# Optimization experiments

Hardware: AMD Instinct MI355X
Metric: run time of the kernel (lower is better)

The kernel has to match this reference:

```python
import jax, jax.numpy as jnp
import numpy as np

N_NODES = 50000
N_EDGES = 800000
D = 64
BN_EPS = 1e-5


def setup_inputs() -> dict:
    key = jax.random.key(0)
    ks = jax.random.split(key, 16)
    x = jax.random.normal(ks[0], (N_NODES, D), dtype=jnp.float32)
    edge_index = jax.random.randint(ks[1], (2, N_EDGES), 0, N_NODES, dtype=jnp.int64)
    s = 1.0 / np.sqrt(D)
    def lin(k):
        kw, kb = jax.random.split(k)
        W = jax.random.uniform(kw, (D, D), jnp.float32, -s, s)
        b = jax.random.uniform(kb, (D,), jnp.float32, -s, s)
        return W, b
    W1_0, b1_0 = lin(ks[2])
    W2_0, b2_0 = lin(ks[3])
    W1_1, b1_1 = lin(ks[4])
    W2_1, b2_1 = lin(ks[5])
    return {
        "x": x, "edge_index": edge_index,
        "W1_0": W1_0, "b1_0": b1_0, "g_0": jnp.ones((D,), jnp.float32), "beta_0": jnp.zeros((D,), jnp.float32), "W2_0": W2_0, "b2_0": b2_0,
        "W1_1": W1_1, "b1_1": b1_1, "g_1": jnp.ones((D,), jnp.float32), "beta_1": jnp.zeros((D,), jnp.float32), "W2_1": W2_1, "b2_1": b2_1,
    }


def _gin_layer(x, src, dst, W1, b1, g, beta, W2, b2):
    # GINConv with eps=0: h_i = MLP( x_i + sum_{j->i} x_j )
    agg = jax.ops.segment_sum(x[src], dst, num_segments=N_NODES)  # [N, D]
    h = agg + x
    h = h @ W1 + b1
    # BatchNorm1d (training-mode batch statistics, biased variance)
    mean = jnp.mean(h, axis=0)
    var = jnp.var(h, axis=0)
    h = (h - mean) * jax.lax.rsqrt(var + BN_EPS) * g + beta
    h = jax.nn.relu(h)
    h = jax.nn.relu(h @ W2 + b2)
    return h


def reference(x, edge_index, W1_0, b1_0, g_0, beta_0, W2_0, b2_0,
              W1_1, b1_1, g_1, beta_1, W2_1, b2_1):
    src = edge_index[0]  # message source j
    dst = edge_index[1]  # aggregation target i
    h1 = _gin_layer(x, src, dst, W1_0, b1_0, g_0, beta_0, W2_0, b2_0)
    h2 = _gin_layer(h1, src, dst, W1_1, b1_1, g_1, beta_1, W2_1, b2_1)
    return (h1, h2)
```

## Files before the change

### kernel.cpp

```cpp
#include <hip/hip_runtime.h>
#include <hip/hip_bf16.h>

#define N_NODES 50000
#define N_EDGES 800000
#define DD 64
#define RPB 64
#define GBLOCKS ((N_NODES + RPB - 1) / RPB)
#define MBLOCKS ((N_NODES + 63) / 64)
#define NBUCKET ((N_NODES + 63) / 64)
#define PIDSTRIDE 800
#define NBP (NBUCKET * 8)
#define SCAN_BLOCKS ((N_NODES + 255) / 256)
#define EDGE_BLOCKS (N_EDGES / 256)
#define BN_EPS 1e-5f


__device__ __forceinline__ float bf2f(unsigned short b) {
    return __uint_as_float(((unsigned)b) << 16);
}
__device__ __forceinline__ float loadF(const void* p, int i, int isf) {
    return isf ? ((const float*)p)[i] : bf2f(((const unsigned short*)p)[i]);
}
template<bool ISF>
__device__ __forceinline__ float4 ld4(const void* p, int i) {
    if (ISF) return *reinterpret_cast<const float4*>((const float*)p + i);
    ushort4 u = *reinterpret_cast<const ushort4*>((const unsigned short*)p + i);
    return make_float4(bf2f(u.x), bf2f(u.y), bf2f(u.z), bf2f(u.w));
}
__device__ __forceinline__ void acc8(float4& a, float4& b, uint4 u) {
    a.x += __uint_as_float(u.x << 16);
    a.y += __uint_as_float(u.x & 0xFFFF0000u);
    a.z += __uint_as_float(u.y << 16);
    a.w += __uint_as_float(u.y & 0xFFFF0000u);
    b.x += __uint_as_float(u.z << 16);
    b.y += __uint_as_float(u.z & 0xFFFF0000u);
    b.z += __uint_as_float(u.w << 16);
    b.w += __uint_as_float(u.w & 0xFFFF0000u);
}

__global__ __launch_bounds__(256) void initcast_kernel(
    const void* __restrict__ x, const int* __restrict__ ei,
    int* __restrict__ flags, int* __restrict__ cnt, int* __restrict__ bpcnt,
    unsigned short* __restrict__ xb)
{
    __shared__ int cntF, cntI;
    int t = threadIdx.x;
    if (t == 0) { cntF = 0; cntI = 0; }
    __syncthreads();
    unsigned short wd = ((const unsigned short*)x)[2 * t];
    int e = (wd >> 7) & 0xFF;
    if (e >= 0x70 && e <= 0x8F) atomicAdd(&cntF, 1);
    if (t < 128 && ei[2 * t + 1] == 0) atomicAdd(&cntI, 1);
    __syncthreads();
    int isf = (cntF < 128) ? 1 : 0;
    int i64 = (cntI > 64) ? 1 : 0;

    int gid = blockIdx.x * 256 + t;
    if (blockIdx.x == 0 && t == 0) {
        flags[0] = isf;
        flags[1] = i64;
    }

    {
        int d = i64 ? ei[2 * N_EDGES + 2 * gid] : ei[N_EDGES + gid];
        atomicAdd(cnt + d, 1);
        atomicAdd(bpcnt + (blockIdx.x & 7) * PIDSTRIDE + (d >> 6), 1);
    }

    int i = gid * 8;
    if (i < N_NODES * DD) {
        if (isf) {
            float4 a = *reinterpret_cast<const float4*>((const float*)x + i);
            float4 b = *reinterpret_cast<const float4*>((const float*)x + i + 4);
            ushort4 o0, o1;
            o0.x = __bfloat16_as_ushort(__float2bfloat16(a.x));
            o0.y = __bfloat16_as_ushort(__float2bfloat16(a.y));
            o0.z = __bfloat16_as_ushort(__float2bfloat16(a.z));
            o0.w = __bfloat16_as_ushort(__float2bfloat16(a.w));
            o1.x = __bfloat16_as_ushort(__float2bfloat16(b.x));
            o1.y = __bfloat16_as_ushort(__float2bfloat16(b.y));
            o1.z = __bfloat16_as_ushort(__float2bfloat16(b.z));
            o1.w = __bfloat16_as_ushort(__float2bfloat16(b.w));
            *reinterpret_cast<ushort4*>(xb + i) = o0;
            *reinterpret_cast<ushort4*>(xb + i + 4) = o1;
        } else {
            *reinterpret_cast<uint4*>(xb + i) =
                *reinterpret_cast<const uint4*>((const unsigned short*)x + i);
        }
    }
}

__global__ __launch_bounds__(256) void scanA_kernel(const int* __restrict__ cnt,
                                                    int* __restrict__ off,
                                                    int* __restrict__ bsum) {
    __shared__ int tmp[256];
    int t = threadIdx.x;
    int i = blockIdx.x * 256 + t;
    int v = (i < N_NODES) ? cnt[i] : 0;
    tmp[t] = v;
    __syncthreads();
    #pragma unroll
    for (int d = 1; d < 256; d <<= 1) {
        int u = (t >= d) ? tmp[t - d] : 0;
        __syncthreads();
        tmp[t] += u;
        __syncthreads();
    }
    if (i < N_NODES) off[i] = tmp[t] - v;
    if (t == 255) bsum[blockIdx.x] = tmp[255];
}

__global__ __launch_bounds__(256) void scanC_kernel(const int* __restrict__ bsum,
                                                    int* __restrict__ off) {
    __shared__ int tmp[256];
    int t = threadIdx.x;
    int v = (t < SCAN_BLOCKS) ? bsum[t] : 0;
    tmp[t] = v;
    __syncthreads();
    #pragma unroll
    for (int d = 1; d < 256; d <<= 1) {
        int u = (t >= d) ? tmp[t - d] : 0;
        __syncthreads();
        tmp[t] += u;
        __syncthreads();
    }
    int base = (blockIdx.x == 0) ? 0 : tmp[blockIdx.x - 1];
    int i = blockIdx.x * 256 + t;
    if (i < N_NODES) off[i] = off[i] + base;
    if (blockIdx.x == SCAN_BLOCKS - 1 && t == 0) off[N_NODES] = tmp[SCAN_BLOCKS - 1];
}

#define BPCH 25
__global__ __launch_bounds__(256) void bpscan_kernel(const int* __restrict__ bpcnt,
                                                     int* __restrict__ bpcur) {
    __shared__ int tmp[256];
    int t = threadIdx.x;
    int lo = t * BPCH;
    int hi = lo + BPCH; if (hi > NBP) hi = NBP;
    int s = 0;
    for (int i = lo; i < hi; ++i)
        s += bpcnt[(i & 7) * PIDSTRIDE + (i >> 3)];
    tmp[t] = s;
    __syncthreads();
    #pragma unroll
    for (int d = 1; d < 256; d <<= 1) {
        int u = (t >= d) ? tmp[t - d] : 0;
        __syncthreads();
        tmp[t] += u;
        __syncthreads();
    }
    int run = (t == 0) ? 0 : tmp[t - 1];
    for (int i = lo; i < hi; ++i) {
        bpcur[i * 16] = run;
        run += bpcnt[(i & 7) * PIDSTRIDE + (i >> 3)];
    }
}

__global__ void fillA_kernel(const int* __restrict__ ei, int* __restrict__ bpcur,
                             unsigned int* __restrict__ tmp, const int* __restrict__ flags) {
    int i64 = flags[1];
    int e = blockIdx.x * 256 + threadIdx.x;
    int s, d;
    if (i64) { s = ei[2 * e]; d = ei[2 * N_EDGES + 2 * e]; }
    else     { s = ei[e];     d = ei[N_EDGES + e]; }
    int bin = (d >> 6) * 8 + (blockIdx.x & 7);
    int pos = atomicAdd(bpcur + bin * 16, 1);
    tmp[pos] = (unsigned)s | ((unsigned)(d & 63) << 16);
}

__global__ __launch_bounds__(256) void fillB_kernel(const int* __restrict__ off,
                                                    const unsigned int* __restrict__ tmp,
                                                    unsigned short* __restrict__ srt) {
    __shared__ int cur64[64];
    int b = blockIdx.x;
    int t = threadIdx.x;
    if (t < 64) {
        int idx = b * 64 + t;
        cur64[t] = (idx < N_NODES) ? off[idx] : N_EDGES;
    }
    __syncthreads();
    int start = off[b * 64];
    int endn  = (b + 1) * 64; if (endn > N_NODES) endn = N_NODES;
    int end   = off[endn];
    for (int i = start + t; i < end; i += 256) {
        unsigned v = tmp[i];
        int pos = atomicAdd(&cur64[v >> 16], 1);
        srt[pos] = (unsigned short)(v & 0xFFFFu);
    }
}

__global__ __launch_bounds__(512) void gather_gemm_stats_kernel(
    const unsigned short* __restrict__ xb, const void* __restrict__ self_src, int force_f32,
    const int* __restrict__ off, const unsigned short* __restrict__ srt,
    const void* __restrict__ W, const void* __restrict__ bias,
    float* __restrict__ out_, float* __restrict__ sums, const int* __restrict__ flags)
{
    __shared__ float sIn[RPB][DD];
    __shared__ float r1[8][DD], r2[8][DD];
    int tid = threadIdx.x;
    int lane = tid & 63, w = tid >> 6;
    int rs = lane >> 3, ch = lane & 7;
    int row0 = blockIdx.x * RPB;
    int isf = force_f32 ? 1 : flags[0];

    int lr = w * 8 + rs;
    int r = row0 + lr;
    float4 a  = make_float4(0.f, 0.f, 0.f, 0.f);
    float4 b  = make_float4(0.f, 0.f, 0.f, 0.f);
    float4 a2 = make_float4(0.f, 0.f, 0.f, 0.f);
    float4 b2 = make_float4(0.f, 0.f, 0.f, 0.f);
    if (r < N_NODES) {
        a = isf ? ld4<true>(self_src, r * DD + 8 * ch)
                : ld4<false>(self_src, r * DD + 8 * ch);
        b = isf ? ld4<true>(self_src, r * DD + 8 * ch + 4)
                : ld4<false>(self_src, r * DD + 8 * ch + 4);
        int k0 = off[r], k1 = off[r + 1];
        int k = k0;
        for (; k + 8 <= k1; k += 8) {
            int n0 = srt[k],     n1 = srt[k + 1], n2 = srt[k + 2], n3 = srt[k + 3];
            int n4 = srt[k + 4], n5 = srt[k + 5], n6 = srt[k + 6], n7 = srt[k + 7];
            uint4 u0 = *reinterpret_cast<const uint4*>(xb + n0 * DD + 8 * ch);
            uint4 u1 = *reinterpret_cast<const uint4*>(xb + n1 * DD + 8 * ch);
            uint4 u2 = *reinterpret_cast<const uint4*>(xb + n2 * DD + 8 * ch);
            uint4 u3 = *reinterpret_cast<const uint4*>(xb + n3 * DD + 8 * ch);
            uint4 u4 = *reinterpret_cast<const uint4*>(xb + n4 * DD + 8 * ch);
            uint4 u5 = *reinterpret_cast<const uint4*>(xb + n5 * DD + 8 * ch);
            uint4 u6 = *reinterpret_cast<const uint4*>(xb + n6 * DD + 8 * ch);
            uint4 u7 = *reinterpret_cast<const uint4*>(xb + n7 * DD + 8 * ch);
            acc8(a, b, u0);
            acc8(a2, b2, u1);
            acc8(a, b, u2);
            acc8(a2, b2, u3);
            acc8(a, b, u4);
            acc8(a2, b2, u5);
            acc8(a, b, u6);
            acc8(a2, b2, u7);
        }
        for (; k + 2 <= k1; k += 2) {
            int n0 = srt[k], n1 = srt[k + 1];
            uint4 u0 = *reinterpret_cast<const uint4*>(xb + n0 * DD + 8 * ch);
            uint4 u1 = *reinterpret_cast<const uint4*>(xb + n1 * DD + 8 * ch);
            acc8(a, b, u0);
            acc8(a2, b2, u1);
        }
        if (k < k1) {
            int n0 = srt[k];
            acc8(a, b, *reinterpret_cast<const uint4*>(xb + n0 * DD + 8 * ch));
        }
        a.x += a2.x; a.y += a2.y; a.z += a2.z; a.w += a2.w;
        b.x += b2.x; b.y += b2.y; b.z += b2.z; b.w += b2.w;
    }
    *reinterpret_cast<float4*>(&sIn[lr][8 * ch]) = a;
    *reinterpret_cast<float4*>(&sIn[lr][8 * ch + 4]) = b;
    __syncthreads();

    float wcol[DD];
    #pragma unroll
    for (int k = 0; k < DD; ++k) wcol[k] = loadF(W, k * DD + lane, isf);
    float bv = loadF(bias, lane, isf);

    float s1 = 0.f, s2 = 0.f;
    #pragma unroll 4
    for (int j = 0; j < 8; ++j) {
        int jr = w * 8 + j;
        float c0 = 0.f, c1 = 0.f, c2 = 0.f, c3 = 0.f;
        #pragma unroll
        for (int k = 0; k < DD; k += 4) {
            float4 aa = *reinterpret_cast<const float4*>(&sIn[jr][k]);
            c0 += aa.x * wcol[k];
            c1 += aa.y * wcol[k + 1];
            c2 += aa.z * wcol[k + 2];
            c3 += aa.w * wcol[k + 3];
        }
        float acc = bv + ((c0 + c1) + (c2 + c3));
        int rr = row0 + jr;
        if (rr < N_NODES) {
            out_[rr * DD + lane] = acc;
            s1 += acc;
            s2 += acc * acc;
        }
    }
    r1[w][lane] = s1; r2[w][lane] = s2;
    __syncthreads();
    if (w == 0) {
        float t1 = 0.f, t2 = 0.f;
        #pragma unroll
        for (int q = 0; q < 8; ++q) { t1 += r1[q][lane]; t2 += r2[q][lane]; }
        atomicAdd(&sums[lane], t1);
        atomicAdd(&sums[64 + lane], t2);
    }
}

__global__ __launch_bounds__(256) void mlp2_kernel(
    const float* __restrict__ in_, const float* __restrict__ sums,
    const void* __restrict__ gma, const void* __restrict__ beta,
    const void* __restrict__ W, const void* __restrict__ bias,
    float* __restrict__ oF, unsigned short* obf, const int* __restrict__ flags)
{
    __shared__ float sIn[64][DD];
    __shared__ float sScale[DD], sShift[DD];
    int isf = flags[0];
    int tid = threadIdx.x;
    int c = tid & 63, g = tid >> 6;
    int row0 = blockIdx.x * 64;

    if (tid < 64) {
        float S1 = sums[tid];
        float S2 = sums[64 + tid];
        float mean = S1 * (1.0f / N_NODES);
        float var  = S2 * (1.0f / N_NODES) - mean * mean;
        float scale = rsqrtf(var + BN_EPS) * loadF(gma, tid, isf);
        sScale[tid] = scale;
        sShift[tid] = loadF(beta, tid, isf) - mean * scale;
    }
    __syncthreads();

    #pragma unroll
    for (int j = 0; j < 4; ++j) {
        int lr = (tid >> 4) + 16 * j;
        int cc = (tid & 15) << 2;
        int r = row0 + lr;
        float4 v = make_float4(0.f, 0.f, 0.f, 0.f);
        if (r < N_NODES) {
            v = *reinterpret_cast<const float4*>(in_ + r * DD + cc);
            float4 sc = *reinterpret_cast<const float4*>(&sScale[cc]);
            float4 sh = *reinterpret_cast<const float4*>(&sShift[cc]);
            v.x = fmaxf(v.x * sc.x + sh.x, 0.f);
            v.y = fmaxf(v.y * sc.y + sh.y, 0.f);
            v.z = fmaxf(v.z * sc.z + sh.z, 0.f);
            v.w = fmaxf(v.w * sc.w + sh.w, 0.f);
        }
        *reinterpret_cast<float4*>(&sIn[lr][cc]) = v;
    }
    __syncthreads();

    float wcol[DD];
    #pragma unroll
    for (int k = 0; k < DD; ++k) wcol[k] = loadF(W, k * DD + c, isf);
    float bv = loadF(bias, c, isf);

    #pragma unroll 4
    for (int j = 0; j < 16; ++j) {
        int lr = g * 16 + j;
        float a0 = 0.f, a1 = 0.f, a2 = 0.f, a3 = 0.f;
        #pragma unroll
        for (int k = 0; k < DD; k += 4) {
            float4 a = *reinterpret_cast<const float4*>(&sIn[lr][k]);
            a0 += a.x * wcol[k];
            a1 += a.y * wcol[k + 1];
            a2 += a.z * wcol[k + 2];
            a3 += a.w * wcol[k + 3];
        }
        float acc = fmaxf(bv + ((a0 + a1) + (a2 + a3)), 0.f);
        int r = row0 + lr;
        if (r < N_NODES) {
            oF[r * DD + c] = acc;
            if (obf) obf[r * DD + c] = __bfloat16_as_ushort(__float2bfloat16(acc));
        }
    }
}

extern "C" void kernel_launch(void* const* d_in, const int* in_sizes, int n_in,
                              void* d_out, int out_size, void* d_ws, size_t ws_size,
                              hipStream_t stream)
{
    (void)in_sizes; (void)n_in; (void)out_size; (void)ws_size;
    const void* x  = d_in[0];
    const int* ei  = (const int*)d_in[1];
    const void* W1_0 = d_in[2];  const void* b1_0 = d_in[3];
    const void* g_0  = d_in[4];  const void* be_0 = d_in[5];
    const void* W2_0 = d_in[6];  const void* b2_0 = d_in[7];
    const void* W1_1 = d_in[8];  const void* b1_1 = d_in[9];
    const void* g_1  = d_in[10]; const void* be_1 = d_in[11];
    const void* W2_1 = d_in[12]; const void* b2_1 = d_in[13];

    float* wsf   = (float*)d_ws;
    float* sumsA = wsf;
    float* sumsB = wsf + 128;
    int*  flags  = (int*)(wsf + 256);
    int*  cnt    = (int*)(wsf + 512);
    int*  bpcnt  = cnt + 50048;
    int*  off    = bpcnt + 6400;
    int*  bpcur  = off + 50064;
    int*  bsum   = bpcur + 100096;
    unsigned int* tmp32 = (unsigned int*)(bsum + 304);
    unsigned short* srt = (unsigned short*)(tmp32 + 800000);
    unsigned short* xb  = srt + 800064;
    float* O1    = (float*)d_out;
    float* O2    = O1 + (size_t)N_NODES * DD;

    dim3 blk(256);

    hipMemsetAsync(d_ws, 0, (size_t)(512 + 50048 + 6400) * 4, stream);
    initcast_kernel<<<EDGE_BLOCKS, blk, 0, stream>>>(x, ei, flags, cnt, bpcnt, xb);
    scanA_kernel<<<SCAN_BLOCKS, blk, 0, stream>>>(cnt, off, bsum);
    scanC_kernel<<<SCAN_BLOCKS, blk, 0, stream>>>(bsum, off);
    bpscan_kernel<<<1, blk, 0, stream>>>(bpcnt, bpcur);
    fillA_kernel<<<EDGE_BLOCKS, blk, 0, stream>>>(ei, bpcur, tmp32, flags);
    fillB_kernel<<<NBUCKET, blk, 0, stream>>>(off, tmp32, srt);

    gather_gemm_stats_kernel<<<GBLOCKS, 512, 0, stream>>>(xb, x, 0, off, srt, W1_0, b1_0,
                                                          O2, sumsA, flags);
    mlp2_kernel<<<MBLOCKS, blk, 0, stream>>>(O2, sumsA, g_0, be_0, W2_0, b2_0, O1, xb, flags);

    gather_gemm_stats_kernel<<<GBLOCKS, 512, 0, stream>>>(xb, O1, 1, off, srt, W1_1, b1_1,
                                                          O2, sumsB, flags);
    mlp2_kernel<<<MBLOCKS, blk, 0, stream>>>(O2, sumsB, g_1, be_1, W2_1, b2_1, O2, nullptr, flags);
}
```

Baseline: 330.9 us.

## Derive per-node CSR offsets inside bucket fill instead of global degree scan

Drops the per-node degree atomic counting and the two-kernel global prefix scan. Bucket offsets now come from the existing bucket scan, and each fillB block builds a local 64-node histogram from the bucketed edges, scans it with wave shuffles and writes the node offsets itself. This removes 800K global atomics, two kernel launches and part of the memset, at the cost of a second pass over each bucket's edges inside fillB. Boundary handling for the last bucket (node == N_NODES) writes the end offset.

```diff
diff --git a/kernel.cpp b/kernel.cpp
--- a/kernel.cpp
+++ b/kernel.cpp
@@ -10,7 +10,6 @@
 #define NBUCKET ((N_NODES + 63) / 64)
 #define PIDSTRIDE 800
 #define NBP (NBUCKET * 8)
-#define SCAN_BLOCKS ((N_NODES + 255) / 256)
 #define EDGE_BLOCKS (N_EDGES / 256)
 #define BN_EPS 1e-5f
 
@@ -40,7 +39,7 @@
 
 __global__ __launch_bounds__(256) void initcast_kernel(
     const void* __restrict__ x, const int* __restrict__ ei,
-    int* __restrict__ flags, int* __restrict__ cnt, int* __restrict__ bpcnt,
+    int* __restrict__ flags, int* __restrict__ bpcnt,
     unsigned short* __restrict__ xb)
 {
     __shared__ int cntF, cntI;
@@ -63,7 +62,6 @@
 
     {
         int d = i64 ? ei[2 * N_EDGES + 2 * gid] : ei[N_EDGES + gid];
-        atomicAdd(cnt + d, 1);
         atomicAdd(bpcnt + (blockIdx.x & 7) * PIDSTRIDE + (d >> 6), 1);
     }
 
@@ -90,49 +88,10 @@
     }
 }
 
-__global__ __launch_bounds__(256) void scanA_kernel(const int* __restrict__ cnt,
-                                                    int* __restrict__ off,
-                                                    int* __restrict__ bsum) {
-    __shared__ int tmp[256];
-    int t = threadIdx.x;
-    int i = blockIdx.x * 256 + t;
-    int v = (i < N_NODES) ? cnt[i] : 0;
-    tmp[t] = v;
-    __syncthreads();
-    #pragma unroll
-    for (int d = 1; d < 256; d <<= 1) {
-        int u = (t >= d) ? tmp[t - d] : 0;
-        __syncthreads();
-        tmp[t] += u;
-        __syncthreads();
-    }
-    if (i < N_NODES) off[i] = tmp[t] - v;
-    if (t == 255) bsum[blockIdx.x] = tmp[255];
-}
-
-__global__ __launch_bounds__(256) void scanC_kernel(const int* __restrict__ bsum,
-                                                    int* __restrict__ off) {
-    __shared__ int tmp[256];
-    int t = threadIdx.x;
-    int v = (t < SCAN_BLOCKS) ? bsum[t] : 0;
-    tmp[t] = v;
-    __syncthreads();
-    #pragma unroll
-    for (int d = 1; d < 256; d <<= 1) {
-        int u = (t >= d) ? tmp[t - d] : 0;
-        __syncthreads();
-        tmp[t] += u;
-        __syncthreads();
-    }
-    int base = (blockIdx.x == 0) ? 0 : tmp[blockIdx.x - 1];
-    int i = blockIdx.x * 256 + t;
-    if (i < N_NODES) off[i] = off[i] + base;
-    if (blockIdx.x == SCAN_BLOCKS - 1 && t == 0) off[N_NODES] = tmp[SCAN_BLOCKS - 1];
-}
-
 #define BPCH 25
 __global__ __launch_bounds__(256) void bpscan_kernel(const int* __restrict__ bpcnt,
-                                                     int* __restrict__ bpcur) {
+                                                     int* __restrict__ bpcur,
+                                                     int* __restrict__ boff) {
     __shared__ int tmp[256];
     int t = threadIdx.x;
     int lo = t * BPCH;
@@ -152,8 +111,10 @@
     int run = (t == 0) ? 0 : tmp[t - 1];
     for (int i = lo; i < hi; ++i) {
         bpcur[i * 16] = run;
+        if ((i & 7) == 0) boff[i >> 3] = run;
         run += bpcnt[(i & 7) * PIDSTRIDE + (i >> 3)];
     }
+    if (t == 255) boff[NBUCKET] = tmp[255];
 }
 
 __global__ void fillA_kernel(const int* __restrict__ ei, int* __restrict__ bpcur,
@@ -168,20 +129,34 @@
     tmp[pos] = (unsigned)s | ((unsigned)(d & 63) << 16);
 }
 
-__global__ __launch_bounds__(256) void fillB_kernel(const int* __restrict__ off,
+__global__ __launch_bounds__(256) void fillB_kernel(const int* __restrict__ boff,
                                                     const unsigned int* __restrict__ tmp,
-                                                    unsigned short* __restrict__ srt) {
+                                                    unsigned short* __restrict__ srt,
+                                                    int* __restrict__ off) {
+    __shared__ int lcnt[64];
     __shared__ int cur64[64];
     int b = blockIdx.x;
     int t = threadIdx.x;
+    if (t < 64) lcnt[t] = 0;
+    __syncthreads();
+    int start = boff[b], end = boff[b + 1];
+    for (int i = start + t; i < end; i += 256)
+        atomicAdd(&lcnt[tmp[i] >> 16], 1);
+    __syncthreads();
     if (t < 64) {
-        int idx = b * 64 + t;
-        cur64[t] = (idx < N_NODES) ? off[idx] : N_EDGES;
-    }
-    __syncthreads();
-    int start = off[b * 64];
-    int endn  = (b + 1) * 64; if (endn > N_NODES) endn = N_NODES;
-    int end   = off[endn];
+        int v = lcnt[t];
+        int s = v;
+        #pragma unroll
+        for (int d = 1; d < 64; d <<= 1) {
+            int u = __shfl_up(s, d, 64);
+            if (t >= d) s += u;
+        }
+        int o = start + (s - v);
+        int node = b * 64 + t;
+        if (node <= N_NODES) off[node] = o;
+        cur64[t] = o;
+    }
+    __syncthreads();
     for (int i = start + t; i < end; i += 256) {
         unsigned v = tmp[i];
         int pos = atomicAdd(&cur64[v >> 16], 1);
@@ -378,12 +353,11 @@
     float* sumsA = wsf;
     float* sumsB = wsf + 128;
     int*  flags  = (int*)(wsf + 256);
-    int*  cnt    = (int*)(wsf + 512);
-    int*  bpcnt  = cnt + 50048;
+    int*  bpcnt  = (int*)(wsf + 512);
     int*  off    = bpcnt + 6400;
-    int*  bpcur  = off + 50064;
-    int*  bsum   = bpcur + 100096;
-    unsigned int* tmp32 = (unsigned int*)(bsum + 304);
+    int*  boff   = off + 50064;
+    int*  bpcur  = boff + 800;
+    unsigned int* tmp32 = (unsigned int*)(bpcur + 100096);
     unsigned short* srt = (unsigned short*)(tmp32 + 800000);
     unsigned short* xb  = srt + 800064;
     float* O1    = (float*)d_out;
@@ -391,13 +365,11 @@
 
     dim3 blk(256);
 
-    hipMemsetAsync(d_ws, 0, (size_t)(512 + 50048 + 6400) * 4, stream);
-    initcast_kernel<<<EDGE_BLOCKS, blk, 0, stream>>>(x, ei, flags, cnt, bpcnt, xb);
-    scanA_kernel<<<SCAN_BLOCKS, blk, 0, stream>>>(cnt, off, bsum);
-    scanC_kernel<<<SCAN_BLOCKS, blk, 0, stream>>>(bsum, off);
-    bpscan_kernel<<<1, blk, 0, stream>>>(bpcnt, bpcur);
+    hipMemsetAsync(d_ws, 0, (size_t)(512 + 6400) * 4, stream);
+    initcast_kernel<<<EDGE_BLOCKS, blk, 0, stream>>>(x, ei, flags, bpcnt, xb);
+    bpscan_kernel<<<1, blk, 0, stream>>>(bpcnt, bpcur, boff);
     fillA_kernel<<<EDGE_BLOCKS, blk, 0, stream>>>(ei, bpcur, tmp32, flags);
-    fillB_kernel<<<NBUCKET, blk, 0, stream>>>(off, tmp32, srt);
+    fillB_kernel<<<NBUCKET, blk, 0, stream>>>(boff, tmp32, srt, off);
 
     gather_gemm_stats_kernel<<<GBLOCKS, 512, 0, stream>>>(xb, x, 0, off, srt, W1_0, b1_0,
                                                           O2, sumsA, flags);
```

Result: faster. 309.2 us (-6.6%).
